# Kernel tuning notes

Measured on AMD Instinct MI355X. Metric: run time of the kernel, lower is better.

## Reference

```python
import jax, jax.numpy as jnp
import numpy as np
from jax import lax

T, B, E, H, V, TAGS = 256, 64, 1024, 1024, 50000, 50


def setup_inputs() -> dict:
    key = jax.random.key(0)
    ks = jax.random.split(key, 16)
    s = 0.02
    return {
        "X": jax.random.randint(ks[0], (T, B), 0, V),
        "lengths": jnp.full((B,), T, dtype=jnp.int64 if jax.config.jax_enable_x64 else jnp.int32),
        "embedding": jax.random.normal(ks[1], (V, E), dtype=jnp.float32) * s,
        "w_ih": jax.random.normal(ks[2], (H, E), dtype=jnp.float32) * s,
        "w_hh": jax.random.normal(ks[3], (H, H), dtype=jnp.float32) * s,
        "w_ch": jax.random.normal(ks[4], (H, H), dtype=jnp.float32) * s,
        "w_c2h": jax.random.normal(ks[5], (H, H), dtype=jnp.float32) * s,
        "b_ih": jax.random.normal(ks[6], (H,), dtype=jnp.float32) * s,
        "b_hh": jax.random.normal(ks[7], (H,), dtype=jnp.float32) * s,
        "b_ch": jax.random.normal(ks[8], (H,), dtype=jnp.float32) * s,
        "b_c2h": jax.random.normal(ks[9], (H,), dtype=jnp.float32) * s,
        "dense_w": jax.random.normal(ks[10], (TAGS, H), dtype=jnp.float32) * s,
        "dense_b": jax.random.normal(ks[11], (TAGS,), dtype=jnp.float32) * s,
        "h0": jax.random.normal(ks[12], (B, H), dtype=jnp.float32),
        "c0": jax.random.normal(ks[13], (B, H), dtype=jnp.float32),
    }


def reference(X, lengths, embedding, w_ih, w_hh, w_ch, w_c2h,
              b_ih, b_hh, b_ch, b_c2h, dense_w, dense_b, h0, c0):
    # Embedding lookup: X is time-major [T, B] -> emb [T, B, E]
    emb = embedding[X]

    def step(carry, x_t):
        hx, cx = carry
        pre = x_t @ w_ih.T + b_ih + hx @ w_hh.T + b_hh          # [B, H]
        # In the source, ingate and forgetgate are identical expressions
        gate_if = jax.nn.sigmoid(pre + cx @ w_ch.T + b_ch)
        cellgate = jnp.tanh(pre)
        cy = gate_if * cx + gate_if * cellgate
        outgate = jax.nn.sigmoid(pre + cy @ w_c2h.T + b_c2h)
        hy = outgate * jnp.tanh(cy)
        return (hy, cy), hy

    _, out = lax.scan(step, (h0, c0), emb)                       # out: [T, B, H]
    flat = out.reshape(-1, out.shape[-1])                        # [T*B, H]
    # dropout_rate=0 / eval mode -> identity
    logits = flat @ dense_w.T + dense_b                          # [T*B, TAGS]
    return jax.nn.softmax(logits, axis=1)
```

## Files before the change

### kernel.cpp

```cpp
#include <hip/hip_runtime.h>
#include <hip/hip_cooperative_groups.h>

typedef __bf16 bf16;
typedef __bf16 bf16x8 __attribute__((ext_vector_type(8)));
typedef float f32x4 __attribute__((ext_vector_type(4)));
typedef unsigned int u32;
typedef unsigned long long u64;
typedef unsigned int u32x4 __attribute__((ext_vector_type(4)));

#define TT 256
#define NTAGS 50

#define OFF_WIH   0ull
#define OFF_WHH   2097152ull
#define OFF_WCH   4194304ull
#define OFF_WC2H  6291456ull
#define OFF_DW    8388608ull
#define OFF_XW    8519680ull
#define OFF_HISTB 42074112ull
#define OFF_HB    75628544ull
#define OFF_CB    75890688ull
#define OFF_BAR   76152832ull
#define N_FLAG_WORDS (4 * 64 * 32)

__device__ __forceinline__ u64 cohload(const u64* p) {
  return __hip_atomic_load(p, __ATOMIC_RELAXED, __HIP_MEMORY_SCOPE_AGENT);
}
__device__ __forceinline__ void cohstore(u64* p, u64 v) {
  __hip_atomic_store(p, v, __ATOMIC_RELAXED, __HIP_MEMORY_SCOPE_AGENT);
}
__device__ __forceinline__ bf16x8 cohload_v8(const bf16* p) {
  union { u64 q[2]; bf16x8 v; } u;
  const u64* q = (const u64*)p;
  u.q[0] = cohload(q);
  u.q[1] = cohload(q + 1);
  return u.v;
}
__device__ __forceinline__ u32x4 cohload_q4(const bf16* p) {
  union { u64 q[2]; u32x4 v; } u;
  const u64* q = (const u64*)p;
  u.q[0] = cohload(q);
  u.q[1] = cohload(q + 1);
  return u.v;
}

__global__ void k_prep(const float* __restrict__ wih, const float* __restrict__ whh,
                       const float* __restrict__ wch, const float* __restrict__ wc2h,
                       const float* __restrict__ dw, const float* __restrict__ h0,
                       const float* __restrict__ c0, char* __restrict__ ws) {
  const long N_W = 4194304, N_DW = 65536, N_S = 65536;
  const long TOT = N_W + N_DW + 2 * N_S + N_FLAG_WORDS;
  long stride = (long)gridDim.x * blockDim.x;
  for (long idx = (long)blockIdx.x * blockDim.x + threadIdx.x; idx < TOT; idx += stride) {
    if (idx < N_W) {
      long m = idx >> 20, e = idx & 1048575;
      const float* s = (m == 0) ? wih : (m == 1) ? whh : (m == 2) ? wch : wc2h;
      ((bf16*)(ws + OFF_WIH))[idx] = (bf16)s[e];
    } else if (idx < N_W + N_DW) {
      long j = idx - N_W; long r = j >> 10, e = j & 1023;
      ((bf16*)(ws + OFF_DW))[j] = (bf16)((r < NTAGS) ? dw[r * 1024 + e] : 0.f);
    } else if (idx < N_W + N_DW + N_S) {
      long j = idx - N_W - N_DW;
      ((bf16*)(ws + OFF_HB))[j] = (bf16)h0[j];
    } else if (idx < N_W + N_DW + 2 * N_S) {
      long j = idx - N_W - N_DW - N_S;
      ((bf16*)(ws + OFF_CB))[j] = (bf16)c0[j];
    } else {
      long j = idx - N_W - N_DW - 2 * N_S;
      ((u32*)(ws + OFF_BAR))[j] = 0u;
    }
  }
}

__global__ __launch_bounds__(256, 1) void k_xw(const int* __restrict__ X,
                                               const float* __restrict__ emb,
                                               const float* __restrict__ b_ih,
                                               const float* __restrict__ b_hh,
                                               char* __restrict__ ws) {
  const bf16* wih = (const bf16*)(ws + OFF_WIH);
  bf16* xw = (bf16*)(ws + OFF_XW);
  int l = threadIdx.x & 63, wv = threadIdx.x >> 6;
  int i0 = blockIdx.x * 64 + wv * 16;
  const float* ap = emb + (long)X[i0 + (l & 15)] * 1024 + ((l >> 4) * 8);

  bf16x8 a_reg[32];
#pragma unroll
  for (int k = 0; k < 32; ++k) {
    f32x4 f0 = *(const f32x4*)(ap + k * 32);
    f32x4 f1 = *(const f32x4*)(ap + k * 32 + 4);
    bf16x8 a;
#pragma unroll
    for (int q = 0; q < 4; ++q) { a[q] = (bf16)f0[q]; a[4 + q] = (bf16)f1[q]; }
    a_reg[k] = a;
  }

  f32x4 zero = {0.f, 0.f, 0.f, 0.f};
  for (int ct = 0; ct < 16; ++ct) {
    int h0 = ct * 64;
    const bf16* bp = wih + (long)(h0 + (l & 15)) * 1024 + ((l >> 4) * 8);
    f32x4 acc[4] = {zero, zero, zero, zero};
#pragma unroll
    for (int k = 0; k < 32; ++k)
#pragma unroll
      for (int j = 0; j < 4; ++j) {
        bf16x8 b = *(const bf16x8*)(bp + j * 16 * 1024 + k * 32);
        acc[j] = __builtin_amdgcn_mfma_f32_16x16x32_bf16(a_reg[k], b, acc[j], 0, 0, 0);
      }
#pragma unroll
    for (int j = 0; j < 4; ++j)
#pragma unroll
      for (int r = 0; r < 4; ++r) {
        int row = i0 + (l >> 4) * 4 + r;
        int col = h0 + j * 16 + (l & 15);
        xw[(long)row * 1024 + col] = (bf16)(acc[j][r] + b_ih[col] + b_hh[col]);
      }
  }
}

__global__ __launch_bounds__(256, 1) void k_rnn(const float* __restrict__ b_ch,
                                                const float* __restrict__ b_c2h,
                                                const float* __restrict__ c0,
                                                char* __restrict__ ws) {
  const bf16* xw = (const bf16*)(ws + OFF_XW);
  bf16* histb = (bf16*)(ws + OFF_HISTB);
  bf16* HB = (bf16*)(ws + OFF_HB);
  bf16* CB = (bf16*)(ws + OFF_CB);
  int g = blockIdx.x & 3, j = blockIdx.x >> 2;
  u32* flags = (u32*)(ws + OFF_BAR) + g * 64 * 32;

  int l = threadIdx.x & 63, wv = threadIdx.x >> 6;
  int b0 = g * 16, h0b = j * 16;
  int e = threadIdx.x;
  int eoff = (b0 + (e >> 4)) * 1024 + h0b + (e & 15);
  int gh = h0b + (e & 15);

  __shared__ float red[4][2][256];
  __shared__ bf16 xfer[256];

  int lane_r = l & 15;
  int koff = wv * 256 + ((l >> 4) * 8);
  long arow = (long)(b0 + lane_r) * 1024 + koff;

  u32x4 whh_r[8], wch_r[8], wc2h_r[8], cfr[8];
  {
    const bf16* p1 = (const bf16*)(ws + OFF_WHH)  + (long)(h0b + lane_r) * 1024 + koff;
    const bf16* p2 = (const bf16*)(ws + OFF_WCH)  + (long)(h0b + lane_r) * 1024 + koff;
    const bf16* p3 = (const bf16*)(ws + OFF_WC2H) + (long)(h0b + lane_r) * 1024 + koff;
#pragma unroll
    for (int kk = 0; kk < 8; ++kk) {
      whh_r[kk]  = *(const u32x4*)(p1 + kk * 32);
      wch_r[kk]  = *(const u32x4*)(p2 + kk * 32);
      wc2h_r[kk] = *(const u32x4*)(p3 + kk * 32);
      cfr[kk] = cohload_q4(CB + arow + kk * 32);
    }
  }

  float bch_v = b_ch[gh], bc2h_v = b_c2h[gh];
  float c_reg = c0[eoff];
  f32x4 zero = {0.f, 0.f, 0.f, 0.f};

  for (int t = 0; t < TT; ++t) {
    asm volatile("" : "+v"(whh_r[0]), "+v"(whh_r[1]), "+v"(whh_r[2]), "+v"(whh_r[3]),
                      "+v"(whh_r[4]), "+v"(whh_r[5]), "+v"(whh_r[6]), "+v"(whh_r[7]),
                      "+v"(wch_r[0]), "+v"(wch_r[1]), "+v"(wch_r[2]), "+v"(wch_r[3]),
                      "+v"(wch_r[4]), "+v"(wch_r[5]), "+v"(wch_r[6]), "+v"(wch_r[7]));
    asm volatile("" : "+v"(wc2h_r[0]), "+v"(wc2h_r[1]), "+v"(wc2h_r[2]), "+v"(wc2h_r[3]),
                      "+v"(wc2h_r[4]), "+v"(wc2h_r[5]), "+v"(wc2h_r[6]), "+v"(wc2h_r[7]));
    asm volatile("" : "+v"(cfr[0]), "+v"(cfr[1]), "+v"(cfr[2]), "+v"(cfr[3]),
                      "+v"(cfr[4]), "+v"(cfr[5]), "+v"(cfr[6]), "+v"(cfr[7]));

    long slot1 = (long)((t + 1) & 1) * 65536;
    float xwv = (float)xw[(long)t * 65536 + eoff];
    u32 tkA = 2u * t + 1u, tkB = 2u * t + 2u;
    const bf16* hx = HB + (long)(t & 1) * 65536;

    f32x4 ap_ = zero, ac_ = zero;
#pragma unroll
    for (int kk = 0; kk < 8; ++kk) {
      bf16x8 a1 = cohload_v8(hx + arow + kk * 32);
      ap_ = __builtin_amdgcn_mfma_f32_16x16x32_bf16(
          a1, __builtin_bit_cast(bf16x8, whh_r[kk]), ap_, 0, 0, 0);
      ac_ = __builtin_amdgcn_mfma_f32_16x16x32_bf16(
          __builtin_bit_cast(bf16x8, cfr[kk]), __builtin_bit_cast(bf16x8, wch_r[kk]), ac_, 0, 0, 0);
    }
#pragma unroll
    for (int r = 0; r < 4; ++r) {
      int ei = ((l >> 4) * 4 + r) * 16 + (l & 15);
      red[wv][0][ei] = ap_[r];
      red[wv][1][ei] = ac_[r];
    }
    __syncthreads();
    float pre = red[0][0][e] + red[1][0][e] + red[2][0][e] + red[3][0][e] + xwv;
    float cgm = red[0][1][e] + red[1][1][e] + red[2][1][e] + red[3][1][e] + bch_v;
    float gif = 1.f / (1.f + expf(-(pre + cgm)));
    float cy = gif * (c_reg + tanhf(pre));
    c_reg = cy;
    xfer[e] = (bf16)cy;
    __syncthreads();
    if (e < 64)
      cohstore((u64*)(CB + slot1 + (long)(b0 + (e >> 2)) * 1024 + h0b) + (e & 3),
               ((u64*)xfer)[e]);
    asm volatile("s_waitcnt vmcnt(0)" ::: "memory");
    if (e == 0)
      __hip_atomic_store(&flags[j * 32], tkA, __ATOMIC_RELAXED, __HIP_MEMORY_SCOPE_AGENT);
    if (e < 64) {
      const u32* my = &flags[e * 32];
      while (!__all(__hip_atomic_load(my, __ATOMIC_RELAXED, __HIP_MEMORY_SCOPE_AGENT) >= tkA))
        __builtin_amdgcn_s_sleep(1);
    }
    asm volatile("" ::: "memory");
    __syncthreads();

    f32x4 ao = zero;
#pragma unroll
    for (int kk = 0; kk < 8; ++kk) {
      cfr[kk] = cohload_q4(CB + slot1 + arow + kk * 32);
      ao = __builtin_amdgcn_mfma_f32_16x16x32_bf16(
          __builtin_bit_cast(bf16x8, cfr[kk]), __builtin_bit_cast(bf16x8, wc2h_r[kk]), ao, 0, 0, 0);
    }
#pragma unroll
    for (int r = 0; r < 4; ++r)
      red[wv][0][((l >> 4) * 4 + r) * 16 + (l & 15)] = ao[r];
    __syncthreads();
    float o = red[0][0][e] + red[1][0][e] + red[2][0][e] + red[3][0][e] + bc2h_v;
    float og = 1.f / (1.f + expf(-(pre + o)));
    bf16 hb = (bf16)(og * tanhf(cy));
    xfer[e] = hb;
    __syncthreads();
    if (t < TT - 1) {
      if (e < 64)
        cohstore((u64*)(HB + slot1 + (long)(b0 + (e >> 2)) * 1024 + h0b) + (e & 3),
                 ((u64*)xfer)[e]);
      asm volatile("s_waitcnt vmcnt(0)" ::: "memory");
      if (e == 0)
        __hip_atomic_store(&flags[j * 32], tkB, __ATOMIC_RELAXED, __HIP_MEMORY_SCOPE_AGENT);
      histb[(long)t * 65536 + eoff] = hb;
      if (e < 64) {
        const u32* my = &flags[e * 32];
        while (!__all(__hip_atomic_load(my, __ATOMIC_RELAXED, __HIP_MEMORY_SCOPE_AGENT) >= tkB))
          __builtin_amdgcn_s_sleep(1);
      }
      asm volatile("" ::: "memory");
      __syncthreads();
    } else {
      histb[(long)t * 65536 + eoff] = hb;
    }
  }
}

__global__ __launch_bounds__(256) void k_out(const float* __restrict__ dense_b,
                                             const char* __restrict__ ws,
                                             float* __restrict__ out) {
  const bf16* h  = (const bf16*)(ws + OFF_HISTB);
  const bf16* dw = (const bf16*)(ws + OFF_DW);
  int l = threadIdx.x & 63, wv = threadIdx.x >> 6;
  int i0 = blockIdx.x * 64 + wv * 16;
  const bf16* ap = h  + (long)(i0 + (l & 15)) * 1024 + ((l >> 4) * 8);
  const bf16* bp = dw + (long)(l & 15) * 1024 + ((l >> 4) * 8);
  f32x4 zero = {0.f, 0.f, 0.f, 0.f};
  f32x4 acc[4] = {zero, zero, zero, zero};
  for (int k = 0; k < 1024; k += 32) {
    bf16x8 a = *(const bf16x8*)(ap + k);
#pragma unroll
    for (int j = 0; j < 4; ++j) {
      bf16x8 b = *(const bf16x8*)(bp + j * 16 * 1024 + k);
      acc[j] = __builtin_amdgcn_mfma_f32_16x16x32_bf16(a, b, acc[j], 0, 0, 0);
    }
  }
  int tag0 = l & 15;
#pragma unroll
  for (int r = 0; r < 4; ++r) {
    int row = i0 + (l >> 4) * 4 + r;
    float lg[4], ex[4];
    float mx = -1e30f;
#pragma unroll
    for (int j = 0; j < 4; ++j) {
      int tag = j * 16 + tag0;
      lg[j] = (tag < NTAGS) ? (acc[j][r] + dense_b[tag]) : -1e30f;
      mx = fmaxf(mx, lg[j]);
    }
    for (int m = 1; m < 16; m <<= 1) mx = fmaxf(mx, __shfl_xor(mx, m, 64));
    float s = 0.f;
#pragma unroll
    for (int j = 0; j < 4; ++j) {
      int tag = j * 16 + tag0;
      ex[j] = (tag < NTAGS) ? expf(lg[j] - mx) : 0.f;
      s += ex[j];
    }
    for (int m = 1; m < 16; m <<= 1) s += __shfl_xor(s, m, 64);
    float inv = 1.f / s;
#pragma unroll
    for (int j = 0; j < 4; ++j) {
      int tag = j * 16 + tag0;
      if (tag < NTAGS) out[(long)row * 50 + tag] = ex[j] * inv;
    }
  }
}

extern "C" void kernel_launch(void* const* d_in, const int* in_sizes, int n_in,
                              void* d_out, int out_size, void* d_ws, size_t ws_size,
                              hipStream_t stream) {
  const int*   X        = (const int*)d_in[0];
  const float* embedding = (const float*)d_in[2];
  const float* w_ih  = (const float*)d_in[3];
  const float* w_hh  = (const float*)d_in[4];
  const float* w_ch  = (const float*)d_in[5];
  const float* w_c2h = (const float*)d_in[6];
  const float* b_ih  = (const float*)d_in[7];
  const float* b_hh  = (const float*)d_in[8];
  const float* b_ch  = (const float*)d_in[9];
  const float* b_c2h = (const float*)d_in[10];
  const float* dense_w = (const float*)d_in[11];
  const float* dense_b = (const float*)d_in[12];
  const float* h0 = (const float*)d_in[13];
  const float* c0 = (const float*)d_in[14];
  char* ws = (char*)d_ws;
  float* out = (float*)d_out;

  k_prep<<<2048, 256, 0, stream>>>(w_ih, w_hh, w_ch, w_c2h, dense_w, h0, c0, ws);
  k_xw<<<256, 256, 0, stream>>>(X, embedding, b_ih, b_hh, ws);

  void* args[] = {(void*)&b_ch, (void*)&b_c2h, (void*)&c0, (void*)&ws};
  hipLaunchCooperativeKernel((const void*)k_rnn, dim3(256), dim3(256), args, 0, stream);

  k_out<<<256, 256, 0, stream>>>(dense_b, ws, out);
}
```

Baseline: 2.285 ms.

## Replace group-wide step barriers with per-chunk producer flag waits in LSTM recurrence

Each wave now waits only on the flag of the specific producer block whose 16-column chunk of h or c it is about to load, instead of a whole-group spin plus __syncthreads. The end-of-step barrier on h is removed: consumers check the h flag at the start of the next step, and the c-path MFMAs are interleaved with those waits so compute overlaps the spinning. The goal is to cut per-timestep synchronization latency on the serial recurrence. The trade-off is more flag polling and looser ordering between blocks, which depends on the double-buffered slots staying safe under the allowed skew.

```diff
diff --git a/kernel.cpp b/kernel.cpp
--- a/kernel.cpp
+++ b/kernel.cpp
@@ -28,13 +28,6 @@
 }
 __device__ __forceinline__ void cohstore(u64* p, u64 v) {
   __hip_atomic_store(p, v, __ATOMIC_RELAXED, __HIP_MEMORY_SCOPE_AGENT);
-}
-__device__ __forceinline__ bf16x8 cohload_v8(const bf16* p) {
-  union { u64 q[2]; bf16x8 v; } u;
-  const u64* q = (const u64*)p;
-  u.q[0] = cohload(q);
-  u.q[1] = cohload(q + 1);
-  return u.v;
 }
 __device__ __forceinline__ u32x4 cohload_q4(const bf16* p) {
   union { u64 q[2]; u32x4 v; } u;
@@ -140,6 +133,7 @@
   int lane_r = l & 15;
   int koff = wv * 256 + ((l >> 4) * 8);
   long arow = (long)(b0 + lane_r) * 1024 + koff;
+  int hp = l >> 5;
 
   u32x4 whh_r[8], wch_r[8], wc2h_r[8], cfr[8];
   {
@@ -171,18 +165,28 @@
 
     long slot1 = (long)((t + 1) & 1) * 65536;
     float xwv = (float)xw[(long)t * 65536 + eoff];
+    u32 tkH = 2u * t;
     u32 tkA = 2u * t + 1u, tkB = 2u * t + 2u;
-    const bf16* hx = HB + (long)(t & 1) * 65536;
 
     f32x4 ap_ = zero, ac_ = zero;
-#pragma unroll
-    for (int kk = 0; kk < 8; ++kk) {
-      bf16x8 a1 = cohload_v8(hx + arow + kk * 32);
+    u32x4 hfr[8];
+    {
+      const bf16* hx = HB + (long)(t & 1) * 65536;
+#pragma unroll
+      for (int kk = 0; kk < 8; ++kk) {
+        const u32* fp = &flags[(wv * 16 + kk * 2 + hp) * 32];
+        while (!__all(__hip_atomic_load(fp, __ATOMIC_RELAXED, __HIP_MEMORY_SCOPE_AGENT) >= tkH))
+          __builtin_amdgcn_s_sleep(1);
+        hfr[kk] = cohload_q4(hx + arow + kk * 32);
+        ac_ = __builtin_amdgcn_mfma_f32_16x16x32_bf16(
+            __builtin_bit_cast(bf16x8, cfr[kk]), __builtin_bit_cast(bf16x8, wch_r[kk]), ac_, 0, 0, 0);
+      }
+    }
+    asm volatile("" ::: "memory");
+#pragma unroll
+    for (int kk = 0; kk < 8; ++kk)
       ap_ = __builtin_amdgcn_mfma_f32_16x16x32_bf16(
-          a1, __builtin_bit_cast(bf16x8, whh_r[kk]), ap_, 0, 0, 0);
-      ac_ = __builtin_amdgcn_mfma_f32_16x16x32_bf16(
-          __builtin_bit_cast(bf16x8, cfr[kk]), __builtin_bit_cast(bf16x8, wch_r[kk]), ac_, 0, 0, 0);
-    }
+          __builtin_bit_cast(bf16x8, hfr[kk]), __builtin_bit_cast(bf16x8, whh_r[kk]), ap_, 0, 0, 0);
 #pragma unroll
     for (int r = 0; r < 4; ++r) {
       int ei = ((l >> 4) * 4 + r) * 16 + (l & 15);
@@ -203,21 +207,23 @@
     asm volatile("s_waitcnt vmcnt(0)" ::: "memory");
     if (e == 0)
       __hip_atomic_store(&flags[j * 32], tkA, __ATOMIC_RELAXED, __HIP_MEMORY_SCOPE_AGENT);
-    if (e < 64) {
-      const u32* my = &flags[e * 32];
-      while (!__all(__hip_atomic_load(my, __ATOMIC_RELAXED, __HIP_MEMORY_SCOPE_AGENT) >= tkA))
-        __builtin_amdgcn_s_sleep(1);
+
+    {
+      const bf16* cyp = CB + slot1;
+#pragma unroll
+      for (int kk = 0; kk < 8; ++kk) {
+        const u32* fp = &flags[(wv * 16 + kk * 2 + hp) * 32];
+        while (!__all(__hip_atomic_load(fp, __ATOMIC_RELAXED, __HIP_MEMORY_SCOPE_AGENT) >= tkA))
+          __builtin_amdgcn_s_sleep(1);
+        cfr[kk] = cohload_q4(cyp + arow + kk * 32);
+      }
     }
     asm volatile("" ::: "memory");
-    __syncthreads();
-
     f32x4 ao = zero;
 #pragma unroll
-    for (int kk = 0; kk < 8; ++kk) {
-      cfr[kk] = cohload_q4(CB + slot1 + arow + kk * 32);
+    for (int kk = 0; kk < 8; ++kk)
       ao = __builtin_amdgcn_mfma_f32_16x16x32_bf16(
           __builtin_bit_cast(bf16x8, cfr[kk]), __builtin_bit_cast(bf16x8, wc2h_r[kk]), ao, 0, 0, 0);
-    }
 #pragma unroll
     for (int r = 0; r < 4; ++r)
       red[wv][0][((l >> 4) * 4 + r) * 16 + (l & 15)] = ao[r];
@@ -234,17 +240,8 @@
       asm volatile("s_waitcnt vmcnt(0)" ::: "memory");
       if (e == 0)
         __hip_atomic_store(&flags[j * 32], tkB, __ATOMIC_RELAXED, __HIP_MEMORY_SCOPE_AGENT);
-      histb[(long)t * 65536 + eoff] = hb;
-      if (e < 64) {
-        const u32* my = &flags[e * 32];
-        while (!__all(__hip_atomic_load(my, __ATOMIC_RELAXED, __HIP_MEMORY_SCOPE_AGENT) >= tkB))
-          __builtin_amdgcn_s_sleep(1);
-      }
-      asm volatile("" ::: "memory");
-      __syncthreads();
-    } else {
-      histb[(long)t * 65536 + eoff] = hb;
-    }
+    }
+    histb[(long)t * 65536 + eoff] = hb;
   }
 }
 
```

Result: slower. 2.556 ms (+11.9%).

## Pre-gather embeddings to bf16 and split input projection across 2D grid

Applied to the files above, without the earlier changes.

The embedding gather and bf16 conversion move into the prep kernel, which writes the gathered rows into the history buffer as scratch. The input-projection GEMM now launches a 2D grid with one 64-column tile per block instead of each block looping over all 16 column tiles. The aim is more parallelism and occupancy in the xw GEMM, which previously used only 256 blocks. In exchange, the 32 MB bf16 embedding copy costs an extra write and read pass, and A tiles are reloaded from global memory per column block rather than held in registers.

```diff
diff --git a/kernel.cpp b/kernel.cpp
--- a/kernel.cpp
+++ b/kernel.cpp
@@ -44,12 +44,13 @@
   return u.v;
 }
 
-__global__ void k_prep(const float* __restrict__ wih, const float* __restrict__ whh,
+__global__ void k_prep(const int* __restrict__ X, const float* __restrict__ emb,
+                       const float* __restrict__ wih, const float* __restrict__ whh,
                        const float* __restrict__ wch, const float* __restrict__ wc2h,
                        const float* __restrict__ dw, const float* __restrict__ h0,
                        const float* __restrict__ c0, char* __restrict__ ws) {
-  const long N_W = 4194304, N_DW = 65536, N_S = 65536;
-  const long TOT = N_W + N_DW + 2 * N_S + N_FLAG_WORDS;
+  const long N_W = 4194304, N_DW = 65536, N_EMB = 16777216, N_S = 65536;
+  const long TOT = N_W + N_DW + N_EMB + 2 * N_S + N_FLAG_WORDS;
   long stride = (long)gridDim.x * blockDim.x;
   for (long idx = (long)blockIdx.x * blockDim.x + threadIdx.x; idx < TOT; idx += stride) {
     if (idx < N_W) {
@@ -59,62 +60,51 @@
     } else if (idx < N_W + N_DW) {
       long j = idx - N_W; long r = j >> 10, e = j & 1023;
       ((bf16*)(ws + OFF_DW))[j] = (bf16)((r < NTAGS) ? dw[r * 1024 + e] : 0.f);
-    } else if (idx < N_W + N_DW + N_S) {
-      long j = idx - N_W - N_DW;
+    } else if (idx < N_W + N_DW + N_EMB) {
+      long j = idx - N_W - N_DW; long i = j >> 10, e = j & 1023;
+      ((bf16*)(ws + OFF_HISTB))[j] = (bf16)emb[(long)X[i] * 1024 + e];
+    } else if (idx < N_W + N_DW + N_EMB + N_S) {
+      long j = idx - N_W - N_DW - N_EMB;
       ((bf16*)(ws + OFF_HB))[j] = (bf16)h0[j];
-    } else if (idx < N_W + N_DW + 2 * N_S) {
-      long j = idx - N_W - N_DW - N_S;
+    } else if (idx < N_W + N_DW + N_EMB + 2 * N_S) {
+      long j = idx - N_W - N_DW - N_EMB - N_S;
       ((bf16*)(ws + OFF_CB))[j] = (bf16)c0[j];
     } else {
-      long j = idx - N_W - N_DW - 2 * N_S;
+      long j = idx - N_W - N_DW - N_EMB - 2 * N_S;
       ((u32*)(ws + OFF_BAR))[j] = 0u;
     }
   }
 }
 
-__global__ __launch_bounds__(256, 1) void k_xw(const int* __restrict__ X,
-                                               const float* __restrict__ emb,
-                                               const float* __restrict__ b_ih,
-                                               const float* __restrict__ b_hh,
-                                               char* __restrict__ ws) {
+__global__ __launch_bounds__(256) void k_xw(const float* __restrict__ b_ih,
+                                            const float* __restrict__ b_hh,
+                                            char* __restrict__ ws) {
+  const bf16* embb = (const bf16*)(ws + OFF_HISTB);
   const bf16* wih = (const bf16*)(ws + OFF_WIH);
   bf16* xw = (bf16*)(ws + OFF_XW);
   int l = threadIdx.x & 63, wv = threadIdx.x >> 6;
   int i0 = blockIdx.x * 64 + wv * 16;
-  const float* ap = emb + (long)X[i0 + (l & 15)] * 1024 + ((l >> 4) * 8);
-
-  bf16x8 a_reg[32];
-#pragma unroll
-  for (int k = 0; k < 32; ++k) {
-    f32x4 f0 = *(const f32x4*)(ap + k * 32);
-    f32x4 f1 = *(const f32x4*)(ap + k * 32 + 4);
-    bf16x8 a;
-#pragma unroll
-    for (int q = 0; q < 4; ++q) { a[q] = (bf16)f0[q]; a[4 + q] = (bf16)f1[q]; }
-    a_reg[k] = a;
-  }
-
+  int h0 = blockIdx.y * 64;
+  const bf16* ap = embb + (long)(i0 + (l & 15)) * 1024 + ((l >> 4) * 8);
+  const bf16* bp = wih + (long)(h0 + (l & 15)) * 1024 + ((l >> 4) * 8);
   f32x4 zero = {0.f, 0.f, 0.f, 0.f};
-  for (int ct = 0; ct < 16; ++ct) {
-    int h0 = ct * 64;
-    const bf16* bp = wih + (long)(h0 + (l & 15)) * 1024 + ((l >> 4) * 8);
-    f32x4 acc[4] = {zero, zero, zero, zero};
-#pragma unroll
-    for (int k = 0; k < 32; ++k)
-#pragma unroll
-      for (int j = 0; j < 4; ++j) {
-        bf16x8 b = *(const bf16x8*)(bp + j * 16 * 1024 + k * 32);
-        acc[j] = __builtin_amdgcn_mfma_f32_16x16x32_bf16(a_reg[k], b, acc[j], 0, 0, 0);
-      }
-#pragma unroll
-    for (int j = 0; j < 4; ++j)
-#pragma unroll
-      for (int r = 0; r < 4; ++r) {
-        int row = i0 + (l >> 4) * 4 + r;
-        int col = h0 + j * 16 + (l & 15);
-        xw[(long)row * 1024 + col] = (bf16)(acc[j][r] + b_ih[col] + b_hh[col]);
-      }
-  }
+  f32x4 acc[4] = {zero, zero, zero, zero};
+  for (int k = 0; k < 1024; k += 32) {
+    bf16x8 a = *(const bf16x8*)(ap + k);
+#pragma unroll
+    for (int j = 0; j < 4; ++j) {
+      bf16x8 b = *(const bf16x8*)(bp + j * 16 * 1024 + k);
+      acc[j] = __builtin_amdgcn_mfma_f32_16x16x32_bf16(a, b, acc[j], 0, 0, 0);
+    }
+  }
+#pragma unroll
+  for (int j = 0; j < 4; ++j)
+#pragma unroll
+    for (int r = 0; r < 4; ++r) {
+      int row = i0 + (l >> 4) * 4 + r;
+      int col = h0 + j * 16 + (l & 15);
+      xw[(long)row * 1024 + col] = (bf16)(acc[j][r] + b_ih[col] + b_hh[col]);
+    }
 }
 
 __global__ __launch_bounds__(256, 1) void k_rnn(const float* __restrict__ b_ch,
@@ -317,8 +307,9 @@
   char* ws = (char*)d_ws;
   float* out = (float*)d_out;
 
-  k_prep<<<2048, 256, 0, stream>>>(w_ih, w_hh, w_ch, w_c2h, dense_w, h0, c0, ws);
-  k_xw<<<256, 256, 0, stream>>>(X, embedding, b_ih, b_hh, ws);
+  k_prep<<<4096, 256, 0, stream>>>(X, embedding, w_ih, w_hh, w_ch, w_c2h,
+                                   dense_w, h0, c0, ws);
+  k_xw<<<dim3(256, 16), 256, 0, stream>>>(b_ih, b_hh, ws);
 
   void* args[] = {(void*)&b_ch, (void*)&b_c2h, (void*)&c0, (void*)&ws};
   hipLaunchCooperativeKernel((const void*)k_rnn, dim3(256), dim3(256), args, 0, stream);
```

Result: no change. 2.269 ms (-0.7%).
